# Performance work log

Measured on AMD Instinct MI355X. Metric: run time of the kernel, lower is better.

## Reference

```python
import jax, jax.numpy as jnp
import numpy as np
from jax import lax

FEAT_STRIDE = 16
RATIOS = np.array([0.5, 1.0, 2.0], np.float32)
SCALES = np.array([8.0, 16.0, 32.0], np.float32)
PRE_NMS, POST_NMS = 6000, 300
NMS_THRESH, MIN_SIZE, SCALE = 0.7, 16.0, 1.0


def anchor_base():
    py = px = FEAT_STRIDE / 2.0
    base = np.zeros((9, 4), np.float32)
    for i, r in enumerate(RATIOS):
        for j, s in enumerate(SCALES):
            h = FEAT_STRIDE * s * np.sqrt(r)
            w = FEAT_STRIDE * s * np.sqrt(1.0 / r)
            base[i * 3 + j] = [px - w / 2.0, py - h / 2.0, px + w / 2.0, py + h / 2.0]
    return jnp.asarray(base)


def all_anchors(h, w):
    base = anchor_base()  # (9,4)
    sy = jnp.arange(h, dtype=jnp.float32) * FEAT_STRIDE
    sx = jnp.arange(w, dtype=jnp.float32) * FEAT_STRIDE
    yy, xx = jnp.meshgrid(sy, sx, indexing='ij')
    shift = jnp.stack([xx.ravel(), yy.ravel(), xx.ravel(), yy.ravel()], axis=1)  # (hw,4)
    return (shift[:, None, :] + base[None, :, :]).reshape(-1, 4)  # (hw*9,4)


def conv2d(x, w, b):
    y = lax.conv_general_dilated(x, w, (1, 1), 'SAME',
                                 dimension_numbers=('NCHW', 'OIHW', 'NCHW'))
    return y + b[None, :, None, None]


def loc2bbox(anchor, loc):
    aw = anchor[:, 2] - anchor[:, 0]
    ah = anchor[:, 3] - anchor[:, 1]
    ax = anchor[:, 0] + 0.5 * aw
    ay = anchor[:, 1] + 0.5 * ah
    cx = loc[:, 0] * aw + ax
    cy = loc[:, 1] * ah + ay
    w = jnp.exp(loc[:, 2]) * aw
    h = jnp.exp(loc[:, 3]) * ah
    return jnp.stack([cx - 0.5 * w, cy - 0.5 * h, cx + 0.5 * w, cy + 0.5 * h], axis=1)


def nms_fixed(boxes, scores):
    # top pre_nms by score, then greedy sequential NMS with fixed shapes
    s, order = lax.top_k(scores, PRE_NMS)
    b = boxes[order]
    areas = (b[:, 2] - b[:, 0]) * (b[:, 3] - b[:, 1])
    idx = jnp.arange(PRE_NMS)

    def body(i, keep):
        xx1 = jnp.maximum(b[i, 0], b[:, 0])
        yy1 = jnp.maximum(b[i, 1], b[:, 1])
        xx2 = jnp.minimum(b[i, 2], b[:, 2])
        yy2 = jnp.minimum(b[i, 3], b[:, 3])
        inter = jnp.clip(xx2 - xx1, 0.0) * jnp.clip(yy2 - yy1, 0.0)
        iou = inter / (areas[i] + areas - inter + 1e-9)
        suppress = (iou > NMS_THRESH) & (idx > i) & keep[i]
        return keep & ~suppress

    keep = lax.fori_loop(0, PRE_NMS, body, jnp.isfinite(s))
    vals, sel = lax.top_k(jnp.where(keep, s, -jnp.inf), POST_NMS)
    roi = b[sel]
    return jnp.where(jnp.isfinite(vals)[:, None], roi, 0.0)  # (POST_NMS,4)


def proposal(loc, fg, anchor, img_h, img_w):
    roi = loc2bbox(anchor, loc)
    roi = jnp.stack([jnp.clip(roi[:, 0], 0.0, img_w), jnp.clip(roi[:, 1], 0.0, img_h),
                     jnp.clip(roi[:, 2], 0.0, img_w), jnp.clip(roi[:, 3], 0.0, img_h)], axis=1)
    ms = MIN_SIZE * SCALE
    valid = ((roi[:, 2] - roi[:, 0]) >= ms) & ((roi[:, 3] - roi[:, 1]) >= ms)
    return nms_fixed(roi, jnp.where(valid, fg, -jnp.inf))


def setup_inputs() -> dict:
    key = jax.random.key(0)
    ks = jax.random.split(key, 4)
    return {
        'x': jax.random.normal(ks[0], (8, 512, 50, 76), jnp.float32),
        'conv1_w': jax.random.normal(ks[1], (512, 512, 3, 3), jnp.float32) * 0.01,
        'conv1_b': jnp.zeros((512,), jnp.float32),
        'score_w': jax.random.normal(ks[2], (18, 512, 1, 1), jnp.float32) * 0.01,
        'score_b': jnp.zeros((18,), jnp.float32),
        'loc_w': jax.random.normal(ks[3], (36, 512, 1, 1), jnp.float32) * 0.01,
        'loc_b': jnp.zeros((36,), jnp.float32),
        'img_h': 800,
        'img_w': 1216,
    }


def reference(x, conv1_w, conv1_b, score_w, score_b, loc_w, loc_b, img_h, img_w):
    b, c, h, w = x.shape
    anchor = all_anchors(h, w)  # (h*w*9,4)
    feat = jax.nn.relu(conv2d(x, conv1_w, conv1_b))
    rpn_locs = conv2d(feat, loc_w, loc_b).transpose(0, 2, 3, 1).reshape(b, -1, 4)
    rpn_scores = conv2d(feat, score_w, score_b).transpose(0, 2, 3, 1)
    sm = jax.nn.softmax(rpn_scores.reshape(b, h, w, 9, 2), axis=4)
    fg = sm[..., 1].reshape(b, -1)
    rpn_scores = rpn_scores.reshape(b, -1, 2)
    rois = jax.vmap(lambda l, f: proposal(l, f, anchor, float(img_h), float(img_w)))(rpn_locs, fg)
    rois = rois.reshape(-1, 4)  # (b*POST_NMS,4)
    return rpn_locs, rpn_scores, rois, anchor
```

## Files before the change

### kernel.cpp

```cpp
#include <hip/hip_runtime.h>
#include <stdint.h>
#include <math.h>

typedef unsigned long long u64;
typedef unsigned int u32;
typedef _Float16 half8 __attribute__((ext_vector_type(8)));
typedef float f32x4 __attribute__((ext_vector_type(4)));

#define CC   512
#define HH   50
#define WW2  76
#define PP   3800
#define NB   8
#define NA   34200
#define PRE  6000
#define POST 300
#define MWORDS 96
#define NPAD 8192
#define SCHUNK 1069


__device__ __forceinline__ u32 skey(float f) {
    u32 u = __float_as_uint(f);
    return (u & 0x80000000u) ? ~u : (u | 0x80000000u);
}

__device__ __forceinline__ float4 anchor_at(int p, int a) {
    const float rv[3] = {0.5f, 1.0f, 2.0f};
    const float sv[3] = {8.0f, 16.0f, 32.0f};
    int ri = a / 3, si = a % 3;
    float s16 = 16.0f * sv[si];
    float hh = s16 * sqrtf(rv[ri]);
    float ww = s16 * sqrtf(1.0f / rv[ri]);
    float bx1 = 8.0f - 0.5f * ww, by1 = 8.0f - 0.5f * hh;
    float bx2 = 8.0f + 0.5f * ww, by2 = 8.0f + 0.5f * hh;
    float sx = (float)((p % WW2) * 16);
    float sy = (float)((p / WW2) * 16);
    return make_float4(sx + bx1, sy + by1, sx + bx2, sy + by2);
}

__device__ __forceinline__ int lds_slot(int m, int j) {
    return (((m >> 4) * 64) + ((m & 15) ^ ((4 * (j & 1)) | (8 * (j >> 1)))) + (j << 4)) << 3;
}

__global__ void k_split_x(const float* __restrict__ x, _Float16* __restrict__ xh,
                          _Float16* __restrict__ xl) {
    __shared__ float S[32][33];
    int zim = blockIdx.z;
    int p0 = blockIdx.x * 32, c0 = blockIdx.y * 32;
    int tx = threadIdx.x, ty0 = threadIdx.y;
    const float* xi = x + (size_t)zim * CC * PP;
#pragma unroll
    for (int yy = 0; yy < 32; yy += 8) {
        int cty = c0 + ty0 + yy, ptx = p0 + tx;
        S[ty0 + yy][tx] = (ptx < PP) ? xi[(size_t)cty * PP + ptx] : 0.f;
    }
    __syncthreads();
#pragma unroll
    for (int yy = 0; yy < 32; yy += 8) {
        int p = p0 + ty0 + yy;
        if (p < PP) {
            float v = S[tx][ty0 + yy];
            _Float16 h = (_Float16)v;
            float r = v - (float)h;
            size_t o = (size_t)(zim * PP + p) * 512 + c0 + tx;
            xh[o] = h;
            xl[o] = (_Float16)(r * 2048.0f);
        }
    }
}

__global__ void k_split_w(const float* __restrict__ w, _Float16* __restrict__ wh,
                          _Float16* __restrict__ wl) {
    __shared__ float S[4608];
    int co = blockIdx.x;
    for (int t = threadIdx.x; t < 4608; t += 256) S[t] = w[(size_t)co * 4608 + t];
    __syncthreads();
    int g = co >> 4, nlo = co & 15;
    for (int e = threadIdx.x; e < 4608; e += 256) {
        int cc = e / 9, idx = e - cc * 9;
        float v = S[cc * 9 + idx];
        _Float16 h = (_Float16)v;
        float r = v - (float)h;
        int kk = (cc >> 5) * 9 + idx;
        int lane = ((cc >> 3) & 3) * 16 + nlo;
        int j = cc & 7;
        size_t d = (((size_t)g * 144 + kk) * 64 + lane) * 8 + j;
        wh[d] = h;
        wl[d] = (_Float16)(r * 2048.0f);
    }
}

__global__ void k_split_w2(const float* __restrict__ lw, const float* __restrict__ sw,
                           _Float16* __restrict__ wh2, _Float16* __restrict__ wl2) {
    int row = blockIdx.x, k = threadIdx.x;
    float v = (row < 36) ? lw[row * 512 + k] : (row < 54 ? sw[(row - 36) * 512 + k] : 0.f);
    _Float16 h = (_Float16)v;
    float r = v - (float)h;
    wh2[row * 512 + k] = h;
    wl2[row * 512 + k] = (_Float16)(r * 2048.0f);
}

__global__ __launch_bounds__(256, 2) void k_conv(
    const _Float16* __restrict__ xh, const _Float16* __restrict__ xl,
    const _Float16* __restrict__ whF, const _Float16* __restrict__ wlF,
    const float* __restrict__ bias, _Float16* __restrict__ fh,
    _Float16* __restrict__ fl, int imgbase)
{
    __shared__ _Float16 lds[2 * 8192];
    const int tid = threadIdx.x;
    const int L = blockIdx.x;
    const int X = L & 7, q = L >> 3;
    const int nt = X & 3;
    const int zim = (X >> 2) * 2 + (q >= 30 ? 1 : 0);
    const int mt = q - (q >= 30 ? 30 : 0);
    const int m0 = mt * 128, n0 = nt * 128;
    const _Float16* xhi = xh + (size_t)zim * CC * PP;
    const _Float16* xlo = xl + (size_t)zim * CC * PP;

    const int mA0 = tid >> 2, jA0 = tid & 3;
    const int mA1 = 64 + (tid >> 2);

    f32x4 acc[4][4], acc2[4][4];
#pragma unroll
    for (int i = 0; i < 4; ++i)
#pragma unroll
        for (int j = 0; j < 4; ++j) {
            acc[i][j] = f32x4{0.f, 0.f, 0.f, 0.f};
            acc2[i][j] = f32x4{0.f, 0.f, 0.f, 0.f};
        }

    uint4 pa0h, pa0l, pa1h, pa1l;

    auto ld_a = [&](int m, int idx, int c0, uint4& vh, uint4& vl) {
        int dy = idx / 3 - 1, dx = idx % 3 - 1;
        int p = m0 + m;
        int px = p % 76, py = p / 76;
        bool av = (p < PP) && ((unsigned)(py + dy) < 50u) && ((unsigned)(px + dx) < 76u);
        if (av) {
            size_t off = (size_t)(p + dy * 76 + dx) * 512 + c0 + jA0 * 8;
            vh = *(const uint4*)(xhi + off);
            vl = *(const uint4*)(xlo + off);
        } else {
            vh = make_uint4(0, 0, 0, 0);
            vl = make_uint4(0, 0, 0, 0);
        }
    };
    auto stage_load = [&](int kk) {
        int c9 = kk / 9;
        int idx = kk - c9 * 9;
        int c0 = c9 << 5;
        ld_a(mA0, idx, c0, pa0h, pa0l);
        ld_a(mA1, idx, c0, pa1h, pa1l);
    };
    const int sl0 = lds_slot(mA0, jA0);
    const int sl1 = lds_slot(mA1, jA0);
    auto stage_write = [&](int buf) {
        _Float16* Lp = lds + buf * 8192;
        *(uint4*)(Lp + sl0)        = pa0h;
        *(uint4*)(Lp + 4096 + sl0) = pa0l;
        *(uint4*)(Lp + sl1)        = pa1h;
        *(uint4*)(Lp + 4096 + sl1) = pa1l;
    };

    const int lane = tid & 63, wave = tid >> 6;
    const int wm = wave & 1, wn = wave >> 1;
    const int jr = lane >> 4;
    const int rd_off = (((lane & 15) ^ ((4 * (jr & 1)) | (8 * (jr >> 1)))) + (jr << 4)) << 3;
    const int g0 = nt * 8 + wn * 4;
    const size_t lane8 = (size_t)lane * 8;

    half8 b0h[4], b0l[4], b1h[4], b1l[4];
    auto load_b = [&](int kk, half8* bh_, half8* bl_) {
#pragma unroll
        for (int ni = 0; ni < 4; ++ni) {
            size_t off = (((size_t)(g0 + ni) * 144 + kk) * 64) * 8 + lane8;
            bh_[ni] = *(const half8*)(whF + off);
            bl_[ni] = *(const half8*)(wlF + off);
        }
    };

    auto compute = [&](int buf, const half8* bh, const half8* bl) {
        const _Float16* Lp = lds + buf * 8192;
        half8 ah[4], al[4];
#pragma unroll
        for (int mi = 0; mi < 4; ++mi) {
            int slot = (((wm * 4 + mi) * 64) << 3) + rd_off;
            ah[mi] = *(const half8*)(Lp + slot);
            al[mi] = *(const half8*)(Lp + 4096 + slot);
        }
#pragma unroll
        for (int ni = 0; ni < 4; ++ni) {
#pragma unroll
            for (int mi = 0; mi < 4; ++mi) {
                acc[mi][ni]  = __builtin_amdgcn_mfma_f32_16x16x32_f16(ah[mi], bh[ni], acc[mi][ni], 0, 0, 0);
                acc2[mi][ni] = __builtin_amdgcn_mfma_f32_16x16x32_f16(ah[mi], bl[ni], acc2[mi][ni], 0, 0, 0);
                acc2[mi][ni] = __builtin_amdgcn_mfma_f32_16x16x32_f16(al[mi], bh[ni], acc2[mi][ni], 0, 0, 0);
            }
        }
    };

    stage_load(0);
    stage_write(0);
    load_b(0, b0h, b0l);
    __syncthreads();
    for (int kk = 0; kk < 144; kk += 2) {
        stage_load(kk + 1);
        load_b(kk + 1, b1h, b1l);
        compute(0, b0h, b0l);
        stage_write(1);
        __syncthreads();
        if (kk + 2 < 144) {
            stage_load(kk + 2);
            load_b(kk + 2, b0h, b0l);
        }
        compute(1, b1h, b1l);
        if (kk + 2 < 144) stage_write(0);
        __syncthreads();
    }

    const int qq = lane >> 4, cl = lane & 15;
    const size_t rowbase = (size_t)(imgbase + zim) * PP;
#pragma unroll
    for (int ni = 0; ni < 4; ++ni) {
        int n = n0 + (wn * 4 + ni) * 16 + cl;
        float bs = bias[n];
#pragma unroll
        for (int mi = 0; mi < 4; ++mi) {
            int mb = m0 + (wm * 4 + mi) * 16 + qq * 4;
            if (mb < PP) {
#pragma unroll
                for (int r = 0; r < 4; ++r) {
                    float v = fmaxf(acc[mi][ni][r] + acc2[mi][ni][r] * (1.f / 2048.f) + bs, 0.f);
                    _Float16 h = (_Float16)v;
                    float rr = v - (float)h;
                    size_t o = (rowbase + mb + r) * 512 + n;
                    fh[o] = h;
                    fl[o] = (_Float16)(rr * 2048.0f);
                }
            }
        }
    }
}

__global__ __launch_bounds__(256) void k_hgemm_post(
    const _Float16* __restrict__ fh, const _Float16* __restrict__ fl,
    const _Float16* __restrict__ wh2, const _Float16* __restrict__ wl2,
    const float* __restrict__ lb, const float* __restrict__ sbias,
    const int* __restrict__ imh_p, const int* __restrict__ imw_p,
    float* __restrict__ out0, float* __restrict__ out1,
    float* __restrict__ boxes, float* __restrict__ scores,
    float* __restrict__ out3)
{
    const int img = blockIdx.y;
    const int p0 = blockIdx.x * 64;
    const int wave = threadIdx.x >> 6, lane = threadIdx.x & 63;
    const int q8 = (lane >> 4) * 8;
    int arow = img * PP + p0 + wave * 16 + (lane & 15);
    if (arow >= NB * PP) arow = NB * PP - 1;
    const _Float16* fhp = fh + (size_t)arow * 512 + q8;
    const _Float16* flp = fl + (size_t)arow * 512 + q8;
    const _Float16* bhp = wh2 + (size_t)(lane & 15) * 512 + q8;
    const _Float16* blp = wl2 + (size_t)(lane & 15) * 512 + q8;

    f32x4 acc[4], acc2[4];
#pragma unroll
    for (int j = 0; j < 4; ++j) {
        acc[j] = f32x4{0.f, 0.f, 0.f, 0.f};
        acc2[j] = f32x4{0.f, 0.f, 0.f, 0.f};
    }

#pragma unroll 4
    for (int k0 = 0; k0 < 512; k0 += 32) {
        half8 ah = *(const half8*)(fhp + k0);
        half8 al = *(const half8*)(flp + k0);
#pragma unroll
        for (int nf = 0; nf < 4; ++nf) {
            half8 bh = *(const half8*)(bhp + (size_t)nf * 16 * 512 + k0);
            half8 bl = *(const half8*)(blp + (size_t)nf * 16 * 512 + k0);
            acc[nf]  = __builtin_amdgcn_mfma_f32_16x16x32_f16(ah, bh, acc[nf], 0, 0, 0);
            acc2[nf] = __builtin_amdgcn_mfma_f32_16x16x32_f16(ah, bl, acc2[nf], 0, 0, 0);
            acc2[nf] = __builtin_amdgcn_mfma_f32_16x16x32_f16(al, bh, acc2[nf], 0, 0, 0);
        }
    }

    __shared__ float Ls[64][68];
    const int q = lane >> 4, cl = lane & 15;
#pragma unroll
    for (int nf = 0; nf < 4; ++nf) {
        int n = nf * 16 + cl;
        float bs = (n < 36) ? lb[n] : (n < 54 ? sbias[n - 36] : 0.f);
#pragma unroll
        for (int r = 0; r < 4; ++r) {
            int ml = wave * 16 + q * 4 + r;
            Ls[ml][n] = acc[nf][r] + acc2[nf][r] * (1.f / 2048.f) + bs;
        }
    }
    __syncthreads();

    const float fimh = (float)(*imh_p), fimw = (float)(*imw_p);
    for (int task = threadIdx.x; task < 576; task += 256) {
        int pl = task / 9, a = task - pl * 9;
        int p = p0 + pl;
        if (p >= PP) continue;
        float4 loc = *(const float4*)&Ls[pl][a * 4];
        float2 sc = make_float2(Ls[pl][36 + a * 2], Ls[pl][36 + a * 2 + 1]);
        size_t ai = (size_t)img * NA + (size_t)p * 9 + a;
        *(float4*)&out0[ai * 4] = loc;
        *(float2*)&out1[ai * 2] = sc;
        float mx = fmaxf(sc.x, sc.y);
        float e0 = expf(sc.x - mx), e1 = expf(sc.y - mx);
        float fg = e1 / (e0 + e1);
        float4 an = anchor_at(p, a);
        if (img == 0) ((float4*)out3)[p * 9 + a] = an;
        float aw = an.z - an.x, ah = an.w - an.y;
        float ax = an.x + 0.5f * aw, ay = an.y + 0.5f * ah;
        float cx = loc.x * aw + ax;
        float cy = loc.y * ah + ay;
        float wb = expf(loc.z) * aw, hb = expf(loc.w) * ah;
        float x1 = cx - 0.5f * wb, y1 = cy - 0.5f * hb;
        float x2 = cx + 0.5f * wb, y2 = cy + 0.5f * hb;
        x1 = fminf(fmaxf(x1, 0.f), fimw);
        x2 = fminf(fmaxf(x2, 0.f), fimw);
        y1 = fminf(fmaxf(y1, 0.f), fimh);
        y2 = fminf(fmaxf(y2, 0.f), fimh);
        bool valid = ((x2 - x1) >= 16.0f) && ((y2 - y1) >= 16.0f);
        ((float4*)boxes)[ai] = make_float4(x1, y1, x2, y2);
        scores[ai] = valid ? fg : -INFINITY;
    }
}


__global__ __launch_bounds__(256) void k_sel_hist(
    const float* __restrict__ scores, u32* __restrict__ ghist,
    const u32* __restrict__ gpref, int sh, int pass)
{
    __shared__ u32 wh[4][256];
    const int img = blockIdx.y, blk = blockIdx.x;
    const int tid = threadIdx.x, wv = tid >> 6;
#pragma unroll
    for (int w = 0; w < 4; ++w) wh[w][tid] = 0;
    __syncthreads();
    const u32 pmask = (pass == 0) ? 0u : (0xFFFFFFFFu << (sh + 8));
    const u32 pref = (pass == 0) ? 0u : gpref[img];
    const float4* sc4 = (const float4*)(scores + (size_t)img * NA);
    const int e40 = blk * SCHUNK;
    const int e41 = min(e40 + SCHUNK, NA / 4);
    for (int e4 = e40 + tid; e4 < e41; e4 += 256) {
        float4 s4 = sc4[e4];
        u32 kv[4] = {skey(s4.x), skey(s4.y), skey(s4.z), skey(s4.w)};
#pragma unroll
        for (int v = 0; v < 4; ++v)
            if ((kv[v] & pmask) == pref) atomicAdd(&wh[wv][(kv[v] >> sh) & 255u], 1u);
    }
    __syncthreads();
    u32 s = wh[0][tid] + wh[1][tid] + wh[2][tid] + wh[3][tid];
    if (s) atomicAdd(&ghist[img * 256 + tid], s);
}

__global__ __launch_bounds__(256) void k_sel_scan(
    u32* __restrict__ ghist, u32* __restrict__ gpref, u32* __restrict__ grem,
    int sh, int pass)
{
    __shared__ u32 A[256];
    __shared__ int s_d;
    const int img = blockIdx.x, t = threadIdx.x;
    u32 h = ghist[img * 256 + t];
    A[t] = h;
    if (t == 0) s_d = 0;
    __syncthreads();
    for (int off = 1; off < 256; off <<= 1) {
        u32 v = A[t] + ((t + off < 256) ? A[t + off] : 0u);
        __syncthreads();
        A[t] = v;
        __syncthreads();
    }
    const u32 rem = (pass == 0) ? (u32)PRE : grem[img];
    if (A[t] >= rem) atomicMax(&s_d, t);
    __syncthreads();
    if (t == 0) {
        int d = s_d;
        u32 snext = (d < 255) ? A[d + 1] : 0u;
        u32 pv = (pass == 0) ? 0u : gpref[img];
        gpref[img] = pv | ((u32)d << sh);
        grem[img] = rem - snext;
    }
    ghist[img * 256 + t] = 0;
}

__global__ __launch_bounds__(256) void k_sel_collect(
    const float* __restrict__ scores, const u32* __restrict__ gpref,
    u32* __restrict__ gccnt, u64* __restrict__ arr)
{
    __shared__ u64 lst[4288];
    __shared__ u32 s_c, s_base;
    const int img = blockIdx.y, blk = blockIdx.x;
    const int tid = threadIdx.x, lane = tid & 63;
    if (tid == 0) s_c = 0;
    __syncthreads();
    const u32 T = gpref[img];
    const float4* sc4 = (const float4*)(scores + (size_t)img * NA);
    const int e40 = blk * SCHUNK;
    const int e41 = min(e40 + SCHUNK, NA / 4);
    for (int e4 = e40 + tid; e4 < e41; e4 += 256) {
        float4 s4 = sc4[e4];
        u32 ks[4] = {skey(s4.x), skey(s4.y), skey(s4.z), skey(s4.w)};
#pragma unroll
        for (int v = 0; v < 4; ++v) {
            bool take = ks[v] >= T;
            u64 bal = __ballot(take);
            if (bal) {
                int leader = __builtin_ctzll(bal);
                u32 base = 0;
                if (lane == leader) base = atomicAdd(&s_c, (u32)__popcll(bal));
                base = (u32)__shfl((int)base, leader);
                if (take)
                    lst[base + (u32)__popcll(bal & ((1ull << lane) - 1ull))] =
                        ((u64)ks[v] << 32) | (u64)(~(u32)(e4 * 4 + v));
            }
        }
    }
    __syncthreads();
    if (tid == 0) s_base = atomicAdd(&gccnt[img], s_c);
    __syncthreads();
    const u32 base = s_base, c = s_c;
    u64* ar = arr + (size_t)img * NPAD;
    for (u32 t = tid; t < c; t += 256) {
        u32 pos = base + t;
        if (pos < NPAD) ar[pos] = lst[t];
    }
}

__global__ __launch_bounds__(1024) void k_sel_sort(
    const float* __restrict__ scores, const float4* __restrict__ boxes,
    const u64* __restrict__ arr, const u32* __restrict__ gccnt,
    float* __restrict__ sb, float4* __restrict__ bbs, float* __restrict__ areas)
{
    extern __shared__ u64 dyn[];
    u64* a = dyn;
    const int img = blockIdx.x, tid = threadIdx.x;
    u32 n = gccnt[img]; if (n > NPAD) n = NPAD;
    const u64* ar = arr + (size_t)img * NPAD;
    for (int t = tid; t < NPAD; t += 1024) a[t] = ((u32)t < n) ? ar[t] : 0ull;
    for (u32 size = 2; size <= NPAD; size <<= 1) {
        for (u32 stride = size >> 1; stride > 0; stride >>= 1) {
            __syncthreads();
            for (u32 t2 = tid; t2 < NPAD / 2; t2 += 1024) {
                u32 i = 2 * t2 - (t2 & (stride - 1));
                u32 j = i + stride;
                u64 x = a[i], y = a[j];
                bool desc = ((i & size) == 0);
                if (desc ? (x < y) : (x > y)) { a[i] = y; a[j] = x; }
            }
        }
    }
    __syncthreads();
    const float* sc = scores + (size_t)img * NA;
    for (int t2 = tid; t2 < PRE; t2 += 1024) {
        u64 v = a[t2];
        u32 e = ~(u32)v;
        float s = sc[e];
        float4 bx = boxes[(size_t)img * NA + e];
        sb[img * PRE + t2] = s;
        bbs[img * PRE + t2] = bx;
        areas[img * PRE + t2] = (bx.z - bx.x) * (bx.w - bx.y);
    }
}

__global__ __launch_bounds__(256) void k_mask(
    const float4* __restrict__ bbs, const float* __restrict__ areas,
    u64* __restrict__ mask)
{
    int img = blockIdx.z, iT = blockIdx.x, jT = blockIdx.y;
    if (jT * 256 + 255 <= iT * 64) return;
    int tid = threadIdx.x;
    __shared__ float4 jb[256];
    __shared__ float ja[256];
    int jj = jT * 256 + tid;
    jb[tid] = (jj < PRE) ? bbs[(size_t)img * PRE + jj] : make_float4(0, 0, 0, 0);
    ja[tid] = (jj < PRE) ? areas[img * PRE + jj] : 0.f;
    __syncthreads();
    int i = iT * 64 + (tid & 63);
    int jw = jT * 4 + (tid >> 6);
    if (i >= PRE) return;
    float4 bi = bbs[(size_t)img * PRE + i];
    float ai = areas[img * PRE + i];
    int j0 = (tid >> 6) * 64;
    u64 m = 0;
#pragma unroll 4
    for (int b = 0; b < 64; ++b) {
        int j = jw * 64 + b;
        if (j >= PRE) break;
        if (j > i) {
            float4 bj = jb[j0 + b];
            float xx1 = fmaxf(bi.x, bj.x), yy1 = fmaxf(bi.y, bj.y);
            float xx2 = fminf(bi.z, bj.z), yy2 = fminf(bi.w, bj.w);
            float iw = fmaxf(xx2 - xx1, 0.f), ih2 = fmaxf(yy2 - yy1, 0.f);
            float inter = iw * ih2;
            float iou = inter / (ai + ja[j0 + b] - inter + 1e-9f);
            if (iou > 0.7f) m |= (1ull << b);
        }
    }
    mask[((size_t)img * PRE + i) * MWORDS + jw] = m;
}

__global__ __launch_bounds__(256) void k_scan(
    const float* __restrict__ sb, const float4* __restrict__ bbs,
    const u64* __restrict__ mask, float* __restrict__ out2)
{
    const int img = blockIdx.x;
    const int tid = threadIdx.x;
    const int lane = tid & 63, wv = tid >> 6;
    __shared__ u64 alive[94];
    __shared__ int list[POST];
    __shared__ int s_n;
    __shared__ u64 wred[4];

    for (int j0 = 0; j0 < 94 * 64; j0 += 256) {
        int j = j0 + tid;
        bool al = (j < PRE) && isfinite(sb[(size_t)img * PRE + j]);
        u64 bal = __ballot(al);
        if (lane == 0) alive[(j0 >> 6) + wv] = bal;
    }
    if (tid == 0) s_n = 0;
    __syncthreads();

    const u64* mimg = mask + (size_t)img * PRE * MWORDS;
    for (int w = 0; w < 94; ++w) {
        int n = s_n;
        if (n >= POST) break;
        u64 myrow = 0;
        if (wv == 0) myrow = mimg[(size_t)(w * 64 + lane) * MWORDS + w];
        u64 loc = 0;
        for (int t = tid; t < n; t += 256)
            loc |= mimg[(size_t)list[t] * MWORDS + w];
#pragma unroll
        for (int off = 32; off > 0; off >>= 1)
            loc |= __shfl_down(loc, off);
        if (lane == 0) wred[wv] = loc;
        __syncthreads();
        if (wv == 0) {
            u64 supp = wred[0] | wred[1] | wred[2] | wred[3];
            u64 cur = alive[w] & ~supp;
            u64 keptw = 0;
            while (cur) {
                int b = __builtin_ctzll(cur);
                keptw |= 1ull << b;
                u64 row = __shfl(myrow, b);
                u64 hi = (b >= 63) ? 0ull : (~0ull << (b + 1));
                cur &= ~row & hi;
            }
            if (lane == 0) {
                int nn = n;
                u64 bits = keptw;
                while (bits && nn < POST) {
                    int bb = __builtin_ctzll(bits);
                    bits &= bits - 1;
                    list[nn++] = w * 64 + bb;
                }
                s_n = nn;
            }
        }
        __syncthreads();
    }
    __syncthreads();
    int n = s_n;
    for (int e = tid; e < POST; e += 256) {
        float4 bx = (e < n) ? bbs[(size_t)img * PRE + list[e]] : make_float4(0, 0, 0, 0);
        *(float4*)&out2[((size_t)img * POST + e) * 4] = bx;
    }
}

extern "C" void kernel_launch(void* const* d_in, const int* in_sizes, int n_in,
                              void* d_out, int out_size, void* d_ws, size_t ws_size,
                              hipStream_t stream)
{
    const float* x     = (const float*)d_in[0];
    const float* w1    = (const float*)d_in[1];
    const float* b1    = (const float*)d_in[2];
    const float* sw    = (const float*)d_in[3];
    const float* sbias = (const float*)d_in[4];
    const float* lw    = (const float*)d_in[5];
    const float* lb    = (const float*)d_in[6];
    const int*   imh   = (const int*)d_in[7];
    const int*   imw   = (const int*)d_in[8];
    float* out = (float*)d_out;
    char* ws = (char*)d_ws;

    _Float16* wh2W = (_Float16*)(ws + 0);
    _Float16* wl2W = (_Float16*)(ws + 65536);
    _Float16* whW  = (_Float16*)(ws + 131072);
    _Float16* wlW  = (_Float16*)(ws + 4849664);
    _Float16* xhW  = (_Float16*)(ws + 9568256);
    _Float16* xlW  = (_Float16*)(ws + 25133056);
    float*    boxesW  = (float*)(ws + 17350656);
    float*    scoresW = (float*)(ws + 21728256);
    float*    sbW     = (float*)(ws + 22822656);
    float*    bbsW    = (float*)(ws + 23014656);
    float*    areasW  = (float*)(ws + 23782656);
    _Float16* fhW  = (_Float16*)(ws + 40697856);
    _Float16* flW  = (_Float16*)(ws + 71827456);
    u64*      maskW   = (u64*)(ws + 40697856);
    u32*      ghistW  = (u32*)(ws + 109581056);
    u32*      gccntW  = (u32*)(ws + 109589248);
    u32*      gprefW  = (u32*)(ws + 109589280);
    u32*      gremW   = (u32*)(ws + 109589312);
    u64*      arrW    = (u64*)(ws + 109597440);

    float* out0 = out;
    float* out1 = out + 1094400;
    float* out2 = out + 1641600;
    float* out3 = out + 1651200;

    hipMemsetAsync(ws + 109581056, 0, 8224, stream);

    hipLaunchKernelGGL(k_split_w, dim3(512), dim3(256), 0, stream, w1, whW, wlW);
    hipLaunchKernelGGL(k_split_w2, dim3(64), dim3(512), 0, stream, lw, sw, wh2W, wl2W);
    for (int b = 0; b < 2; ++b) {
        hipLaunchKernelGGL(k_split_x, dim3(119, 16, 4), dim3(32, 8), 0, stream,
                           x + (size_t)b * 4 * CC * PP, xhW, xlW);
        hipLaunchKernelGGL(k_conv, dim3(480), dim3(256), 0, stream,
                           xhW, xlW, whW, wlW, b1, fhW, flW, b * 4);
    }
    hipLaunchKernelGGL(k_hgemm_post, dim3(60, NB), dim3(256), 0, stream,
                       fhW, flW, wh2W, wl2W, lb, sbias, imh, imw,
                       out0, out1, boxesW, scoresW, out3);
    for (int pass = 0; pass < 4; ++pass) {
        int sh = 24 - 8 * pass;
        hipLaunchKernelGGL(k_sel_hist, dim3(8, NB), dim3(256), 0, stream,
                           scoresW, ghistW, gprefW, sh, pass);
        hipLaunchKernelGGL(k_sel_scan, dim3(NB), dim3(256), 0, stream,
                           ghistW, gprefW, gremW, sh, pass);
    }
    hipLaunchKernelGGL(k_sel_collect, dim3(8, NB), dim3(256), 0, stream,
                       scoresW, gprefW, gccntW, arrW);
    hipLaunchKernelGGL(k_sel_sort, dim3(NB), dim3(1024), NPAD * 8, stream,
                       scoresW, (const float4*)boxesW, arrW, gccntW,
                       sbW, (float4*)bbsW, areasW);
    hipLaunchKernelGGL(k_mask, dim3(94, 24, NB), dim3(256), 0, stream,
                       (const float4*)bbsW, areasW, maskW);
    hipLaunchKernelGGL(k_scan, dim3(NB), dim3(256), 0, stream,
                       sbW, (const float4*)bbsW, maskW, out2);
}
```

Before: 906.7 us.

## Split per-image bitonic sort into two half sorts plus merge-path gather

The single 8192-element bitonic sort per image (8 blocks) becomes two independent 4096-element sorts per image (16 blocks), followed by a merge-path kernel that binary-searches each output rank and gathers scores and boxes. This doubles block-level parallelism, cuts the number of sort stages, and halves shared memory per block. In exchange it adds one kernel launch and a global round trip of the sorted halves.

```diff
diff --git a/kernel.cpp b/kernel.cpp
--- a/kernel.cpp
+++ b/kernel.cpp
@@ -17,6 +17,7 @@
 #define POST 300
 #define MWORDS 96
 #define NPAD 8192
+#define SHALF 4096
 #define SCHUNK 1069
 
 
@@ -431,21 +432,21 @@
     }
 }
 
-__global__ __launch_bounds__(1024) void k_sel_sort(
-    const float* __restrict__ scores, const float4* __restrict__ boxes,
-    const u64* __restrict__ arr, const u32* __restrict__ gccnt,
-    float* __restrict__ sb, float4* __restrict__ bbs, float* __restrict__ areas)
-{
-    extern __shared__ u64 dyn[];
-    u64* a = dyn;
-    const int img = blockIdx.x, tid = threadIdx.x;
+__global__ __launch_bounds__(1024) void k_sel_sort2(
+    u64* __restrict__ arr, const u32* __restrict__ gccnt)
+{
+    __shared__ u64 a[SHALF];
+    const int img = blockIdx.y, half = blockIdx.x;
+    const int tid = threadIdx.x;
     u32 n = gccnt[img]; if (n > NPAD) n = NPAD;
-    const u64* ar = arr + (size_t)img * NPAD;
-    for (int t = tid; t < NPAD; t += 1024) a[t] = ((u32)t < n) ? ar[t] : 0ull;
-    for (u32 size = 2; size <= NPAD; size <<= 1) {
+    u64* ar = arr + (size_t)img * NPAD + (size_t)half * SHALF;
+    const int base = half * SHALF;
+    for (int t = tid; t < SHALF; t += 1024)
+        a[t] = ((u32)(base + t) < n) ? ar[t] : 0ull;
+    for (u32 size = 2; size <= SHALF; size <<= 1) {
         for (u32 stride = size >> 1; stride > 0; stride >>= 1) {
             __syncthreads();
-            for (u32 t2 = tid; t2 < NPAD / 2; t2 += 1024) {
+            for (u32 t2 = tid; t2 < SHALF / 2; t2 += 1024) {
                 u32 i = 2 * t2 - (t2 & (stride - 1));
                 u32 j = i + stride;
                 u64 x = a[i], y = a[j];
@@ -455,16 +456,36 @@
         }
     }
     __syncthreads();
+    for (int t = tid; t < SHALF; t += 1024) ar[t] = a[t];
+}
+
+__global__ __launch_bounds__(1024) void k_sel_merge(
+    const float* __restrict__ scores, const float4* __restrict__ boxes,
+    const u64* __restrict__ arr,
+    float* __restrict__ sb, float4* __restrict__ bbs, float* __restrict__ areas)
+{
+    const int img = blockIdx.y;
+    const int t = blockIdx.x * 1024 + threadIdx.x;
+    if (t >= PRE) return;
+    const u64* A = arr + (size_t)img * NPAD;
+    const u64* B = A + SHALF;
+    int lo = (t > SHALF) ? (t - SHALF) : 0;
+    int hi = (t < SHALF) ? t : SHALF;
+    while (lo < hi) {
+        int mid = (lo + hi) >> 1;
+        if (A[mid] > B[t - 1 - mid]) lo = mid + 1; else hi = mid;
+    }
+    const int i = lo, j = t - lo;
+    u64 va = (i < SHALF) ? A[i] : 0ull;
+    u64 vb = (j < SHALF) ? B[j] : 0ull;
+    u64 v = (va > vb) ? va : vb;
+    u32 e = ~(u32)v;
     const float* sc = scores + (size_t)img * NA;
-    for (int t2 = tid; t2 < PRE; t2 += 1024) {
-        u64 v = a[t2];
-        u32 e = ~(u32)v;
-        float s = sc[e];
-        float4 bx = boxes[(size_t)img * NA + e];
-        sb[img * PRE + t2] = s;
-        bbs[img * PRE + t2] = bx;
-        areas[img * PRE + t2] = (bx.z - bx.x) * (bx.w - bx.y);
-    }
+    float s = sc[e];
+    float4 bx = boxes[(size_t)img * NA + e];
+    sb[img * PRE + t] = s;
+    bbs[img * PRE + t] = bx;
+    areas[img * PRE + t] = (bx.z - bx.x) * (bx.w - bx.y);
 }
 
 __global__ __launch_bounds__(256) void k_mask(
@@ -634,8 +655,10 @@
     }
     hipLaunchKernelGGL(k_sel_collect, dim3(8, NB), dim3(256), 0, stream,
                        scoresW, gprefW, gccntW, arrW);
-    hipLaunchKernelGGL(k_sel_sort, dim3(NB), dim3(1024), NPAD * 8, stream,
-                       scoresW, (const float4*)boxesW, arrW, gccntW,
+    hipLaunchKernelGGL(k_sel_sort2, dim3(2, NB), dim3(1024), 0, stream,
+                       arrW, gccntW);
+    hipLaunchKernelGGL(k_sel_merge, dim3((PRE + 1023) / 1024, NB), dim3(1024), 0, stream,
+                       scoresW, (const float4*)boxesW, arrW,
                        sbW, (float4*)bbsW, areasW);
     hipLaunchKernelGGL(k_mask, dim3(94, 24, NB), dim3(256), 0, stream,
                        (const float4*)bbsW, areasW, maskW);
```

After: 863.8 us. 4.7% less time.
